# Kernel optimization log

Measured on AMD Instinct MI355X. Metric: run time of the kernel, lower is better.

## Reference

```python
import jax, jax.numpy as jnp
import numpy as np

N = 50000      # nodes
E = 250000     # edges
D = 256        # in_channels
MSG = 256      # msg_dim
TD = 64        # time encoder out_channels
ED = MSG + TD  # edge_dim = 320
H = 4          # heads
C = 64         # out_channels // heads


def setup_inputs() -> dict:
    key = jax.random.key(0)
    ks = jax.random.split(key, 16)
    s_d = 1.0 / np.sqrt(D)
    s_e = 1.0 / np.sqrt(ED)
    return {
        "x": jax.random.normal(ks[0], (N, D), jnp.float32),
        "last_update": jax.random.uniform(ks[1], (N,), jnp.float32) * 1000.0,
        "t": jax.random.uniform(ks[2], (E,), jnp.float32) * 1000.0,
        "msg": jax.random.normal(ks[3], (E, MSG), jnp.float32),
        "edge_index": jax.random.randint(ks[4], (2, E), 0, N, jnp.int32),
        # TimeEncoder: Linear(1, TD) followed by cos
        "time_w": jax.random.normal(ks[5], (TD,), jnp.float32),
        "time_b": jax.random.normal(ks[6], (TD,), jnp.float32) * 0.1,
        # TransformerConv linears (weights stored [out, in] like torch)
        "Wq": jax.random.normal(ks[7], (H * C, D), jnp.float32) * s_d,
        "bq": jnp.zeros((H * C,), jnp.float32),
        "Wk": jax.random.normal(ks[8], (H * C, D), jnp.float32) * s_d,
        "bk": jnp.zeros((H * C,), jnp.float32),
        "Wv": jax.random.normal(ks[9], (H * C, D), jnp.float32) * s_d,
        "bv": jnp.zeros((H * C,), jnp.float32),
        "We": jax.random.normal(ks[10], (H * C, ED), jnp.float32) * s_e,  # lin_edge, no bias
        "Wskip": jax.random.normal(ks[11], (H * C, D), jnp.float32) * s_d,
        "bskip": jnp.zeros((H * C,), jnp.float32),
    }


def reference(x, last_update, t, msg, edge_index, time_w, time_b,
              Wq, bq, Wk, bk, Wv, bv, We, Wskip, bskip):
    src = edge_index[0]  # j: message source
    dst = edge_index[1]  # i: message target

    # time encoding: cos(Linear(1, TD)(rel_t))
    rel_t = last_update[src] - t                              # [E]
    rel_t_enc = jnp.cos(rel_t[:, None] * time_w[None, :] + time_b)  # [E, TD]
    edge_attr = jnp.concatenate([rel_t_enc, msg], axis=-1)    # [E, ED]

    # TransformerConv (heads=4, concat=True, root_weight=True, beta=False, eval mode)
    q = (x @ Wq.T + bq).reshape(N, H, C)
    k = (x @ Wk.T + bk).reshape(N, H, C)
    v = (x @ Wv.T + bv).reshape(N, H, C)
    e = (edge_attr @ We.T).reshape(E, H, C)

    k_j = k[src] + e                                           # [E, H, C]
    alpha = jnp.einsum('ehc,ehc->eh', q[dst], k_j) / np.sqrt(C)  # [E, H]

    # segment softmax over incoming edges of each target node
    m = jax.ops.segment_max(alpha, dst, num_segments=N)        # [N, H]
    m = jnp.where(jnp.isfinite(m), m, 0.0)
    ex = jnp.exp(alpha - m[dst])                               # [E, H]
    denom = jax.ops.segment_sum(ex, dst, num_segments=N)       # [N, H]
    alpha = ex / (denom[dst] + 1e-16)                          # [E, H]

    out_e = (v[src] + e) * alpha[:, :, None]                   # [E, H, C]
    out = jax.ops.segment_sum(out_e, dst, num_segments=N)      # [N, H, C]
    out = out.reshape(N, H * C) + (x @ Wskip.T + bskip)        # skip connection
    return out
```

## Files before the change

### kernel.cpp

```cpp
#include <hip/hip_runtime.h>
#include <math.h>

#define NN 50000
#define EE 250000

typedef float f32x4 __attribute__((ext_vector_type(4)));
typedef __bf16 bf16x8 __attribute__((ext_vector_type(8)));

static __device__ __forceinline__ ushort f2b(float f) {
    __bf16 h = (__bf16)f;
    return *(ushort*)&h;
}
static __device__ __forceinline__ float b2f(ushort u) {
    return __uint_as_float(((unsigned)u) << 16);
}

typedef __attribute__((address_space(1))) const unsigned int gu32;
typedef __attribute__((address_space(3))) unsigned int lu32;
static __device__ __forceinline__ void gl2lds16(const void* g, void* l) {
    __builtin_amdgcn_global_load_lds((gu32*)g, (lu32*)l, 16, 0, 0);
}

__global__ void k_prep_w(const float* __restrict__ Wq, const float* __restrict__ bq,
                         const float* __restrict__ Wk, const float* __restrict__ bk,
                         const float* __restrict__ Wv, const float* __restrict__ bv,
                         const float* __restrict__ Wskip, const float* __restrict__ bskip,
                         const float* __restrict__ We,
                         ushort* __restrict__ Wnb_sw, ushort* __restrict__ Web_sw,
                         float* __restrict__ bcat) {
    int i = blockIdx.x * 256 + threadIdx.x;
    int st = gridDim.x * 256;
    for (int ch = i; ch < 16 * 2048; ch += st) {
        int tile = ch >> 11, pc = ch & 2047;
        int r = pc >> 5, sc = pc & 31;
        int c = (sc & 24) | ((sc ^ r) & 7);
        int n = tile * 64 + r, sel = n >> 8, o = n & 255;
        const float* W = (sel == 0) ? Wq : (sel == 1) ? Wk : (sel == 2) ? Wv : Wskip;
        const float* src = W + o * 256 + c * 8;
        union { ushort u[8]; uint4 v; } s;
        #pragma unroll
        for (int j = 0; j < 8; ++j) s.u[j] = f2b(src[j]);
        *(uint4*)&Wnb_sw[(size_t)ch * 8] = s.v;
    }
    for (int ch = i; ch < 5 * 2048; ch += st) {
        int ks = ch >> 11, pc = ch & 2047;
        int r = pc >> 3, q = pc & 7;
        int c = q ^ (r & 7);
        const float* src = We + r * 320 + ks * 64 + c * 8;
        union { ushort u[8]; uint4 v; } s;
        #pragma unroll
        for (int j = 0; j < 8; ++j) s.u[j] = f2b(src[j]);
        *(uint4*)&Web_sw[(size_t)ch * 8] = s.v;
    }
    for (int idx = i; idx < 1024; idx += st) {
        int sel = idx >> 8, o = idx & 255;
        const float* b = (sel == 0) ? bq : (sel == 1) ? bk : (sel == 2) ? bv : bskip;
        bcat[idx] = b[o];
    }
}

__global__ void k_zero(unsigned* __restrict__ deg) {
    int i = blockIdx.x * 256 + threadIdx.x;
    if (i < NN) deg[i] = 0u;
}

__global__ void k_hist(const int* __restrict__ ei, unsigned* __restrict__ deg) {
    int i = blockIdx.x * 256 + threadIdx.x;
    if (i < EE) atomicAdd(&deg[ei[EE + i]], 1u);
}

__global__ __launch_bounds__(1024) void k_scan(const unsigned* __restrict__ deg,
                                               unsigned* __restrict__ offs,
                                               unsigned* __restrict__ cursor) {
    __shared__ unsigned part[1024];
    int t = threadIdx.x;
    const int CH = (NN + 1023) / 1024;
    int b0 = t * CH;
    unsigned s = 0;
    for (int i = 0; i < CH; ++i) { int idx = b0 + i; if (idx < NN) s += deg[idx]; }
    part[t] = s;
    __syncthreads();
    for (int d = 1; d < 1024; d <<= 1) {
        unsigned v = (t >= d) ? part[t - d] : 0u;
        __syncthreads();
        part[t] += v;
        __syncthreads();
    }
    unsigned run = (t == 0) ? 0u : part[t - 1];
    for (int i = 0; i < CH; ++i) {
        int idx = b0 + i;
        if (idx < NN) { offs[idx] = run; cursor[idx] = run; run += deg[idx]; }
    }
    if (t == 1023) offs[NN] = EE;
}

__global__ void k_scatter(const int* __restrict__ ei, unsigned* __restrict__ cursor,
                          int* __restrict__ rank) {
    int i = blockIdx.x * 256 + threadIdx.x;
    if (i < EE) {
        unsigned p = atomicAdd(&cursor[ei[EE + i]], 1u);
        rank[i] = (int)p;
    }
}

__global__ __launch_bounds__(256) void k_node_mfma(
        const float* __restrict__ x, const ushort* __restrict__ Wnb_sw,
        const float* __restrict__ bcat,
        ushort* __restrict__ qb, ushort* __restrict__ kb, ushort* __restrict__ vb,
        float* __restrict__ out) {
    __shared__ ushort As[64 * 256];
    __shared__ ushort Bs[64 * 256];
    int tid = threadIdx.x;
    int lane = tid & 63, wid = tid >> 6;
    int wrow = wid >> 1, wcol = wid & 1;
    int li = lane & 15, g = lane >> 4;
    int bm = blockIdx.x, bng = blockIdx.y;
    #pragma unroll
    for (int i = 0; i < 8; ++i) {
        int ch = tid + i * 256;
        int r = ch >> 5, c = ch & 31;
        int row = bm * 64 + r;
        union { ushort u[8]; uint4 v; } s;
        if (row < NN) {
            const float* xr = x + (size_t)row * 256 + c * 8;
            float4 a = *(const float4*)xr;
            float4 b = *(const float4*)(xr + 4);
            s.u[0] = f2b(a.x); s.u[1] = f2b(a.y); s.u[2] = f2b(a.z); s.u[3] = f2b(a.w);
            s.u[4] = f2b(b.x); s.u[5] = f2b(b.y); s.u[6] = f2b(b.z); s.u[7] = f2b(b.w);
        } else {
            s.v = make_uint4(0, 0, 0, 0);
        }
        int sc = (c & 24) | ((c ^ r) & 7);
        *(uint4*)&As[r * 256 + sc * 8] = s.v;
    }
    for (int bn = 0; bn < 8; ++bn) {
        int bng2 = bng * 8 + bn;
        __syncthreads();
        #pragma unroll
        for (int i = 0; i < 8; ++i) {
            int pcb = (i * 4 + wid) * 64;
            gl2lds16(Wnb_sw + ((size_t)bng2 * 2048 + pcb + lane) * 8, &Bs[pcb * 8]);
        }
        __syncthreads();
        f32x4 acc[2][2] = {};
        #pragma unroll
        for (int ks = 0; ks < 8; ++ks) {
            bf16x8 a[2], b[2];
            int c = ks * 4 + g;
            #pragma unroll
            for (int m = 0; m < 2; ++m) {
                int r = wrow * 32 + m * 16 + li;
                int sc = (c & 24) | ((c ^ r) & 7);
                a[m] = *(const bf16x8*)&As[r * 256 + sc * 8];
            }
            #pragma unroll
            for (int n = 0; n < 2; ++n) {
                int r = wcol * 32 + n * 16 + li;
                int sc = (c & 24) | ((c ^ r) & 7);
                b[n] = *(const bf16x8*)&Bs[r * 256 + sc * 8];
            }
            #pragma unroll
            for (int m = 0; m < 2; ++m)
                #pragma unroll
                for (int n = 0; n < 2; ++n)
                    acc[m][n] = __builtin_amdgcn_mfma_f32_16x16x32_bf16(a[m], b[n], acc[m][n], 0, 0, 0);
        }
        int sel = bng2 >> 2;
        int cbase = (bng2 & 3) * 64;
        ushort* dstb = (sel == 0) ? qb : (sel == 1) ? kb : vb;
        #pragma unroll
        for (int m = 0; m < 2; ++m) {
            #pragma unroll
            for (int r = 0; r < 4; ++r) {
                int row = bm * 64 + wrow * 32 + m * 16 + g * 4 + r;
                if (row >= NN) continue;
                #pragma unroll
                for (int n = 0; n < 2; ++n) {
                    int coll = wcol * 32 + n * 16 + li;
                    float val = acc[m][n][r] + bcat[bng2 * 64 + coll];
                    int cin = cbase + coll;
                    if (sel < 3) dstb[(size_t)row * 256 + cin] = f2b(val);
                    else         out[(size_t)row * 256 + cin] = val;
                }
            }
        }
    }
}

__global__ __launch_bounds__(256) void k_edge_mfma(
        const float* __restrict__ msg, const float* __restrict__ t_arr,
        const float* __restrict__ lu, const float* __restrict__ tw,
        const float* __restrict__ tb, const ushort* __restrict__ Web_sw,
        const ushort* __restrict__ qb, const ushort* __restrict__ kb,
        const ushort* __restrict__ vb, const int* __restrict__ ei,
        const int* __restrict__ rank,
        ushort* __restrict__ ebuf, float* __restrict__ alpha) {
    __shared__ ushort SS[64 * 328];
    __shared__ int s_src[64], s_dst[64], s_rank[64];
    __shared__ float s_relt[64];
    int tid = threadIdx.x;
    int lane = tid & 63, wid = tid >> 6;
    int wr = wid >> 1, wc = wid & 1;
    int li = lane & 15, g = lane >> 4;
    int e0 = blockIdx.x * 64;
    if (tid < 64) {
        int e = e0 + tid;
        if (e >= EE) e = EE - 1;
        int s = ei[e];
        s_src[tid] = s;
        s_dst[tid] = ei[EE + e];
        s_rank[tid] = rank[e];
        s_relt[tid] = lu[s] - t_arr[e];
    }
    f32x4 acc[2][8] = {};
    for (int ks = 0; ks < 5; ++ks) {
        int k0 = ks * 64;
        __syncthreads();
        #pragma unroll
        for (int i = 0; i < 8; ++i) {
            int pcb = (i * 4 + wid) * 64;
            gl2lds16(Web_sw + ((size_t)ks * 2048 + pcb + lane) * 8, &SS[4096 + pcb * 8]);
        }
        #pragma unroll
        for (int i = 0; i < 2; ++i) {
            int ch = tid + i * 256;
            int r = ch >> 3, c = ch & 7;
            union { ushort u[8]; uint4 v; } s;
            if (k0 == 0) {
                float rt = s_relt[r];
                #pragma unroll
                for (int j = 0; j < 8; ++j)
                    s.u[j] = f2b(cosf(rt * tw[c * 8 + j] + tb[c * 8 + j]));
            } else {
                int erow = e0 + r; if (erow >= EE) erow = EE - 1;
                const float* mrow = msg + (size_t)erow * 256 + (k0 - 64) + c * 8;
                float4 a = *(const float4*)mrow;
                float4 b = *(const float4*)(mrow + 4);
                s.u[0] = f2b(a.x); s.u[1] = f2b(a.y); s.u[2] = f2b(a.z); s.u[3] = f2b(a.w);
                s.u[4] = f2b(b.x); s.u[5] = f2b(b.y); s.u[6] = f2b(b.z); s.u[7] = f2b(b.w);
            }
            *(uint4*)&SS[r * 64 + ((c ^ (r & 7)) * 8)] = s.v;
        }
        __syncthreads();
        #pragma unroll
        for (int kk = 0; kk < 2; ++kk) {
            bf16x8 a[2], b[8];
            #pragma unroll
            for (int m = 0; m < 2; ++m) {
                int r = wr * 32 + m * 16 + li;
                a[m] = *(const bf16x8*)&SS[r * 64 + (((kk * 4 + g) ^ (r & 7)) * 8)];
            }
            #pragma unroll
            for (int n = 0; n < 8; ++n) {
                int r = wc * 128 + n * 16 + li;
                b[n] = *(const bf16x8*)&SS[4096 + r * 64 + (((kk * 4 + g) ^ (r & 7)) * 8)];
            }
            #pragma unroll
            for (int m = 0; m < 2; ++m)
                #pragma unroll
                for (int n = 0; n < 8; ++n)
                    acc[m][n] = __builtin_amdgcn_mfma_f32_16x16x32_bf16(a[m], b[n], acc[m][n], 0, 0, 0);
        }
    }
    __syncthreads();
    #pragma unroll
    for (int i = 0; i < 8; ++i) {
        int idx = tid + i * 256;
        int r = idx >> 5, c = idx & 31;
        uint4 vv = *(const uint4*)(vb + (size_t)s_src[r] * 256 + c * 8);
        *(uint4*)&SS[r * 328 + c * 8] = vv;
    }
    __syncthreads();
    #pragma unroll
    for (int m = 0; m < 2; ++m) {
        #pragma unroll
        for (int r = 0; r < 4; ++r) {
            int el = wr * 32 + m * 16 + g * 4 + r;
            int edge = e0 + el;
            if (edge >= EE) continue;
            size_t rb = (size_t)s_rank[el] * 256;
            #pragma unroll
            for (int n = 0; n < 8; ++n) {
                int col = wc * 128 + n * 16 + li;
                ebuf[rb + col] = f2b(acc[m][n][r] + b2f(SS[el * 328 + col]));
            }
        }
    }
    __syncthreads();
    #pragma unroll
    for (int i = 0; i < 8; ++i) {
        int idx = tid + i * 256;
        int r = idx >> 5, c = idx & 31;
        uint4 kv = *(const uint4*)(kb + (size_t)s_src[r] * 256 + c * 8);
        *(uint4*)&SS[r * 328 + c * 8] = kv;
    }
    __syncthreads();
    #pragma unroll
    for (int m = 0; m < 2; ++m)
        #pragma unroll
        for (int r = 0; r < 4; ++r) {
            int el = wr * 32 + m * 16 + g * 4 + r;
            #pragma unroll
            for (int n = 0; n < 8; ++n)
                acc[m][n][r] += b2f(SS[el * 328 + wc * 128 + n * 16 + li]);
        }
    __syncthreads();
    #pragma unroll
    for (int i = 0; i < 8; ++i) {
        int idx = tid + i * 256;
        int r = idx >> 5, c = idx & 31;
        uint4 qv = *(const uint4*)(qb + (size_t)s_dst[r] * 256 + c * 8);
        *(uint4*)&SS[r * 328 + c * 8] = qv;
    }
    __syncthreads();
    #pragma unroll
    for (int m = 0; m < 2; ++m) {
        #pragma unroll
        for (int r = 0; r < 4; ++r) {
            int el = wr * 32 + m * 16 + g * 4 + r;
            int edge = e0 + el;
            float p0 = 0.f, p1 = 0.f;
            #pragma unroll
            for (int n = 0; n < 8; ++n) {
                float qv = b2f(SS[el * 328 + wc * 128 + n * 16 + li]);
                float tt = qv * acc[m][n][r];
                if (n < 4) p0 += tt; else p1 += tt;
            }
            #pragma unroll
            for (int msk = 1; msk < 16; msk <<= 1) {
                p0 += __shfl_xor(p0, msk);
                p1 += __shfl_xor(p1, msk);
            }
            if (li < 2 && edge < EE) {
                float av = ((li == 0) ? p0 : p1) * 0.125f;
                int h = wc * 2 + li;
                alpha[(size_t)s_rank[el] * 4 + h] = av;
            }
        }
    }
}

__global__ __launch_bounds__(256) void k_gather(
        const ushort* __restrict__ ebuf, const float* __restrict__ alpha,
        const unsigned* __restrict__ offs, float* __restrict__ out) {
    int wid = threadIdx.x >> 6, lane = threadIdx.x & 63;
    int n = blockIdx.x * 4 + wid;
    if (n >= NN) return;
    unsigned p0 = offs[n], p1 = offs[n + 1];
    if (p0 == p1) return;
    int h = lane >> 4;
    int c0 = lane * 4;
    float m = -INFINITY;
    for (unsigned p = p0; p < p1; ++p)
        m = fmaxf(m, alpha[(size_t)p * 4 + h]);
    f32x4 acc = {0.f, 0.f, 0.f, 0.f};
    float denom = 0.f;
    for (unsigned p = p0; p < p1; ++p) {
        float ex = __expf(alpha[(size_t)p * 4 + h] - m);
        ushort4 ev = *(const ushort4*)(ebuf + (size_t)p * 256 + c0);
        acc[0] += b2f(ev.x) * ex;
        acc[1] += b2f(ev.y) * ex;
        acc[2] += b2f(ev.z) * ex;
        acc[3] += b2f(ev.w) * ex;
        denom += ex;
    }
    float inv = 1.f / (denom + 1e-16f);
    float4 o = *(float4*)(out + (size_t)n * 256 + c0);
    o.x += acc[0] * inv;
    o.y += acc[1] * inv;
    o.z += acc[2] * inv;
    o.w += acc[3] * inv;
    *(float4*)(out + (size_t)n * 256 + c0) = o;
}

extern "C" void kernel_launch(void* const* d_in, const int* in_sizes, int n_in,
                              void* d_out, int out_size, void* d_ws, size_t ws_size,
                              hipStream_t stream) {
    const float* x        = (const float*)d_in[0];
    const float* last_upd = (const float*)d_in[1];
    const float* t_arr    = (const float*)d_in[2];
    const float* msg      = (const float*)d_in[3];
    const int*   ei       = (const int*)d_in[4];
    const float* time_w   = (const float*)d_in[5];
    const float* time_b   = (const float*)d_in[6];
    const float* Wq = (const float*)d_in[7];  const float* bq = (const float*)d_in[8];
    const float* Wk = (const float*)d_in[9];  const float* bk = (const float*)d_in[10];
    const float* Wv = (const float*)d_in[11]; const float* bv = (const float*)d_in[12];
    const float* We = (const float*)d_in[13];
    const float* Wsk = (const float*)d_in[14]; const float* bsk = (const float*)d_in[15];
    float* out = (float*)d_out;
    char* base = (char*)d_ws;

    size_t off = 0;
    auto carve = [&](size_t bytes) {
        void* p = base + off;
        off += (bytes + 255) & ~(size_t)255;
        return p;
    };
    ushort* Wnb_sw = (ushort*)carve((size_t)16 * 2048 * 8 * 2);
    ushort* Web_sw = (ushort*)carve((size_t)5 * 2048 * 8 * 2);
    float*  bcat  = (float*) carve(1024 * 4);
    ushort* qb    = (ushort*)carve((size_t)NN * 256 * 2);
    ushort* kb    = (ushort*)carve((size_t)NN * 256 * 2);
    ushort* vb    = (ushort*)carve((size_t)NN * 256 * 2);
    ushort* ebuf  = (ushort*)carve((size_t)EE * 256 * 2);
    float*  alpha = (float*) carve((size_t)EE * 4 * 4);
    unsigned* deg    = (unsigned*)carve((size_t)NN * 4);
    unsigned* cursor = (unsigned*)carve((size_t)NN * 4);
    unsigned* offs   = (unsigned*)carve((size_t)(NN + 1) * 4);
    int*      rank   = (int*)     carve((size_t)EE * 4);

    k_prep_w<<<dim3(512), dim3(256), 0, stream>>>(Wq, bq, Wk, bk, Wv, bv, Wsk, bsk, We,
                                                  Wnb_sw, Web_sw, bcat);
    k_zero<<<dim3((NN + 255) / 256), dim3(256), 0, stream>>>(deg);
    k_hist<<<dim3((EE + 255) / 256), dim3(256), 0, stream>>>(ei, deg);
    k_scan<<<dim3(1), dim3(1024), 0, stream>>>(deg, offs, cursor);
    k_scatter<<<dim3((EE + 255) / 256), dim3(256), 0, stream>>>(ei, cursor, rank);
    k_node_mfma<<<dim3(782, 2), dim3(256), 0, stream>>>(x, Wnb_sw, bcat, qb, kb, vb, out);
    k_edge_mfma<<<dim3((EE + 63) / 64), dim3(256), 0, stream>>>(
        msg, t_arr, last_upd, time_w, time_b, Web_sw, qb, kb, vb, ei, rank, ebuf, alpha);
    k_gather<<<dim3((NN + 3) / 4), dim3(256), 0, stream>>>(ebuf, alpha, offs, out);
}
```

Baseline: 555.7 us.

## Shrink edge kernel LDS via 32-wide K steps and half-tile gather epilogue

The edge MFMA kernel now steps K in chunks of 32 instead of 64, with the We weight layout and XOR swizzle reworked to match. The epilogue gathers v/k/q rows for 32 edges at a time rather than 64, and only the owning warps consume each half. Together these cut the shared-memory footprint from about 42KB to about 20KB, so more blocks can be resident per CU. The cost is twice as many K-loop barriers and a serialized two-pass epilogue in which half the warps sit idle during each pass.

```diff
diff --git a/kernel.cpp b/kernel.cpp
--- a/kernel.cpp
+++ b/kernel.cpp
@@ -42,11 +42,11 @@
         for (int j = 0; j < 8; ++j) s.u[j] = f2b(src[j]);
         *(uint4*)&Wnb_sw[(size_t)ch * 8] = s.v;
     }
-    for (int ch = i; ch < 5 * 2048; ch += st) {
-        int ks = ch >> 11, pc = ch & 2047;
-        int r = pc >> 3, q = pc & 7;
-        int c = q ^ (r & 7);
-        const float* src = We + r * 320 + ks * 64 + c * 8;
+    for (int ch = i; ch < 10 * 1024; ch += st) {
+        int ks = ch >> 10, pc = ch & 1023;
+        int r = pc >> 2, sc = pc & 3;
+        int c = sc ^ ((r >> 2) & 3);
+        const float* src = We + r * 320 + ks * 32 + c * 8;
         union { ushort u[8]; uint4 v; } s;
         #pragma unroll
         for (int j = 0; j < 8; ++j) s.u[j] = f2b(src[j]);
@@ -195,7 +195,7 @@
         const ushort* __restrict__ vb, const int* __restrict__ ei,
         const int* __restrict__ rank,
         ushort* __restrict__ ebuf, float* __restrict__ alpha) {
-    __shared__ ushort SS[64 * 328];
+    __shared__ ushort SS[10240];
     __shared__ int s_src[64], s_dst[64], s_rank[64];
     __shared__ float s_relt[64];
     int tid = threadIdx.x;
@@ -213,24 +213,23 @@
         s_relt[tid] = lu[s] - t_arr[e];
     }
     f32x4 acc[2][8] = {};
-    for (int ks = 0; ks < 5; ++ks) {
-        int k0 = ks * 64;
-        __syncthreads();
-        #pragma unroll
-        for (int i = 0; i < 8; ++i) {
+    for (int ks = 0; ks < 10; ++ks) {
+        int k0 = ks * 32;
+        __syncthreads();
+        #pragma unroll
+        for (int i = 0; i < 4; ++i) {
             int pcb = (i * 4 + wid) * 64;
-            gl2lds16(Web_sw + ((size_t)ks * 2048 + pcb + lane) * 8, &SS[4096 + pcb * 8]);
-        }
-        #pragma unroll
-        for (int i = 0; i < 2; ++i) {
-            int ch = tid + i * 256;
-            int r = ch >> 3, c = ch & 7;
+            gl2lds16(Web_sw + ((size_t)ks * 1024 + pcb + lane) * 8,
+                     &SS[2048 + pcb * 8]);
+        }
+        {
+            int r = tid >> 2, c = tid & 3;
             union { ushort u[8]; uint4 v; } s;
-            if (k0 == 0) {
+            if (k0 < 64) {
                 float rt = s_relt[r];
                 #pragma unroll
                 for (int j = 0; j < 8; ++j)
-                    s.u[j] = f2b(cosf(rt * tw[c * 8 + j] + tb[c * 8 + j]));
+                    s.u[j] = f2b(cosf(rt * tw[k0 + c * 8 + j] + tb[k0 + c * 8 + j]));
             } else {
                 int erow = e0 + r; if (erow >= EE) erow = EE - 1;
                 const float* mrow = msg + (size_t)erow * 256 + (k0 - 64) + c * 8;
@@ -239,102 +238,110 @@
                 s.u[0] = f2b(a.x); s.u[1] = f2b(a.y); s.u[2] = f2b(a.z); s.u[3] = f2b(a.w);
                 s.u[4] = f2b(b.x); s.u[5] = f2b(b.y); s.u[6] = f2b(b.z); s.u[7] = f2b(b.w);
             }
-            *(uint4*)&SS[r * 64 + ((c ^ (r & 7)) * 8)] = s.v;
-        }
-        __syncthreads();
-        #pragma unroll
-        for (int kk = 0; kk < 2; ++kk) {
-            bf16x8 a[2], b[8];
+            int sc = c ^ ((r >> 2) & 3);
+            *(uint4*)&SS[r * 32 + sc * 8] = s.v;
+        }
+        __syncthreads();
+        bf16x8 a[2], b[8];
+        #pragma unroll
+        for (int m = 0; m < 2; ++m) {
+            int r = wr * 32 + m * 16 + li;
+            a[m] = *(const bf16x8*)&SS[r * 32 + ((g ^ ((r >> 2) & 3)) * 8)];
+        }
+        #pragma unroll
+        for (int n = 0; n < 8; ++n) {
+            int r = wc * 128 + n * 16 + li;
+            b[n] = *(const bf16x8*)&SS[2048 + r * 32 + ((g ^ ((r >> 2) & 3)) * 8)];
+        }
+        #pragma unroll
+        for (int m = 0; m < 2; ++m)
+            #pragma unroll
+            for (int n = 0; n < 8; ++n)
+                acc[m][n] = __builtin_amdgcn_mfma_f32_16x16x32_bf16(a[m], b[n], acc[m][n], 0, 0, 0);
+    }
+    #pragma unroll
+    for (int hh = 0; hh < 2; ++hh) {
+        bool own = (wr == hh);
+        __syncthreads();
+        #pragma unroll
+        for (int i = 0; i < 4; ++i) {
+            int idx = tid + i * 256;
+            int r = idx >> 5, c = idx & 31;
+            uint4 vv = *(const uint4*)(vb + (size_t)s_src[hh * 32 + r] * 256 + c * 8);
+            *(uint4*)&SS[r * 264 + c * 8] = vv;
+        }
+        __syncthreads();
+        if (own) {
             #pragma unroll
             for (int m = 0; m < 2; ++m) {
-                int r = wr * 32 + m * 16 + li;
-                a[m] = *(const bf16x8*)&SS[r * 64 + (((kk * 4 + g) ^ (r & 7)) * 8)];
-            }
-            #pragma unroll
-            for (int n = 0; n < 8; ++n) {
-                int r = wc * 128 + n * 16 + li;
-                b[n] = *(const bf16x8*)&SS[4096 + r * 64 + (((kk * 4 + g) ^ (r & 7)) * 8)];
-            }
+                #pragma unroll
+                for (int r = 0; r < 4; ++r) {
+                    int el = m * 16 + g * 4 + r;
+                    int edge = e0 + hh * 32 + el;
+                    if (edge >= EE) continue;
+                    size_t rb = (size_t)s_rank[hh * 32 + el] * 256;
+                    #pragma unroll
+                    for (int n = 0; n < 8; ++n) {
+                        int col = wc * 128 + n * 16 + li;
+                        ebuf[rb + col] = f2b(acc[m][n][r] + b2f(SS[el * 264 + col]));
+                    }
+                }
+            }
+        }
+        __syncthreads();
+        #pragma unroll
+        for (int i = 0; i < 4; ++i) {
+            int idx = tid + i * 256;
+            int r = idx >> 5, c = idx & 31;
+            uint4 kv = *(const uint4*)(kb + (size_t)s_src[hh * 32 + r] * 256 + c * 8);
+            *(uint4*)&SS[r * 264 + c * 8] = kv;
+        }
+        __syncthreads();
+        if (own) {
             #pragma unroll
             for (int m = 0; m < 2; ++m)
                 #pragma unroll
-                for (int n = 0; n < 8; ++n)
-                    acc[m][n] = __builtin_amdgcn_mfma_f32_16x16x32_bf16(a[m], b[n], acc[m][n], 0, 0, 0);
-        }
-    }
-    __syncthreads();
-    #pragma unroll
-    for (int i = 0; i < 8; ++i) {
-        int idx = tid + i * 256;
-        int r = idx >> 5, c = idx & 31;
-        uint4 vv = *(const uint4*)(vb + (size_t)s_src[r] * 256 + c * 8);
-        *(uint4*)&SS[r * 328 + c * 8] = vv;
-    }
-    __syncthreads();
-    #pragma unroll
-    for (int m = 0; m < 2; ++m) {
-        #pragma unroll
-        for (int r = 0; r < 4; ++r) {
-            int el = wr * 32 + m * 16 + g * 4 + r;
-            int edge = e0 + el;
-            if (edge >= EE) continue;
-            size_t rb = (size_t)s_rank[el] * 256;
-            #pragma unroll
-            for (int n = 0; n < 8; ++n) {
-                int col = wc * 128 + n * 16 + li;
-                ebuf[rb + col] = f2b(acc[m][n][r] + b2f(SS[el * 328 + col]));
-            }
-        }
-    }
-    __syncthreads();
-    #pragma unroll
-    for (int i = 0; i < 8; ++i) {
-        int idx = tid + i * 256;
-        int r = idx >> 5, c = idx & 31;
-        uint4 kv = *(const uint4*)(kb + (size_t)s_src[r] * 256 + c * 8);
-        *(uint4*)&SS[r * 328 + c * 8] = kv;
-    }
-    __syncthreads();
-    #pragma unroll
-    for (int m = 0; m < 2; ++m)
-        #pragma unroll
-        for (int r = 0; r < 4; ++r) {
-            int el = wr * 32 + m * 16 + g * 4 + r;
-            #pragma unroll
-            for (int n = 0; n < 8; ++n)
-                acc[m][n][r] += b2f(SS[el * 328 + wc * 128 + n * 16 + li]);
-        }
-    __syncthreads();
-    #pragma unroll
-    for (int i = 0; i < 8; ++i) {
-        int idx = tid + i * 256;
-        int r = idx >> 5, c = idx & 31;
-        uint4 qv = *(const uint4*)(qb + (size_t)s_dst[r] * 256 + c * 8);
-        *(uint4*)&SS[r * 328 + c * 8] = qv;
-    }
-    __syncthreads();
-    #pragma unroll
-    for (int m = 0; m < 2; ++m) {
-        #pragma unroll
-        for (int r = 0; r < 4; ++r) {
-            int el = wr * 32 + m * 16 + g * 4 + r;
-            int edge = e0 + el;
-            float p0 = 0.f, p1 = 0.f;
-            #pragma unroll
-            for (int n = 0; n < 8; ++n) {
-                float qv = b2f(SS[el * 328 + wc * 128 + n * 16 + li]);
-                float tt = qv * acc[m][n][r];
-                if (n < 4) p0 += tt; else p1 += tt;
-            }
-            #pragma unroll
-            for (int msk = 1; msk < 16; msk <<= 1) {
-                p0 += __shfl_xor(p0, msk);
-                p1 += __shfl_xor(p1, msk);
-            }
-            if (li < 2 && edge < EE) {
-                float av = ((li == 0) ? p0 : p1) * 0.125f;
-                int h = wc * 2 + li;
-                alpha[(size_t)s_rank[el] * 4 + h] = av;
+                for (int r = 0; r < 4; ++r) {
+                    int el = m * 16 + g * 4 + r;
+                    #pragma unroll
+                    for (int n = 0; n < 8; ++n)
+                        acc[m][n][r] += b2f(SS[el * 264 + wc * 128 + n * 16 + li]);
+                }
+        }
+        __syncthreads();
+        #pragma unroll
+        for (int i = 0; i < 4; ++i) {
+            int idx = tid + i * 256;
+            int r = idx >> 5, c = idx & 31;
+            uint4 qv = *(const uint4*)(qb + (size_t)s_dst[hh * 32 + r] * 256 + c * 8);
+            *(uint4*)&SS[r * 264 + c * 8] = qv;
+        }
+        __syncthreads();
+        if (own) {
+            #pragma unroll
+            for (int m = 0; m < 2; ++m) {
+                #pragma unroll
+                for (int r = 0; r < 4; ++r) {
+                    int el = m * 16 + g * 4 + r;
+                    int edge = e0 + hh * 32 + el;
+                    float p0 = 0.f, p1 = 0.f;
+                    #pragma unroll
+                    for (int n = 0; n < 8; ++n) {
+                        float qv = b2f(SS[el * 264 + wc * 128 + n * 16 + li]);
+                        float tt = qv * acc[m][n][r];
+                        if (n < 4) p0 += tt; else p1 += tt;
+                    }
+                    #pragma unroll
+                    for (int msk = 1; msk < 16; msk <<= 1) {
+                        p0 += __shfl_xor(p0, msk);
+                        p1 += __shfl_xor(p1, msk);
+                    }
+                    if (li < 2 && edge < EE) {
+                        float av = ((li == 0) ? p0 : p1) * 0.125f;
+                        int h = wc * 2 + li;
+                        alpha[(size_t)s_rank[hh * 32 + el] * 4 + h] = av;
+                    }
+                }
             }
         }
     }
@@ -398,7 +405,7 @@
         return p;
     };
     ushort* Wnb_sw = (ushort*)carve((size_t)16 * 2048 * 8 * 2);
-    ushort* Web_sw = (ushort*)carve((size_t)5 * 2048 * 8 * 2);
+    ushort* Web_sw = (ushort*)carve((size_t)10 * 1024 * 8 * 2);
     float*  bcat  = (float*) carve(1024 * 4);
     ushort* qb    = (ushort*)carve((size_t)NN * 256 * 2);
     ushort* kb    = (ushort*)carve((size_t)NN * 256 * 2);
```

After: 587.4 us. 5.7% more time.

## Process edges in destination-sorted order and fold degree zeroing into prep

Applied to the files above, without the earlier changes.

The scatter pass now writes per-edge src, dst, original id and relative time into CSR-sorted arrays, so the edge kernel walks edges in destination order. Its ebuf and alpha writes become contiguous, and the q[dst] gathers hit nearby rows. In exchange, msg rows are now read by a scattered original edge id, and the scatter pass writes four arrays instead of one. The separate zeroing kernel is merged into the weight prep kernel to save a launch.

```diff
diff --git a/kernel.cpp b/kernel.cpp
--- a/kernel.cpp
+++ b/kernel.cpp
@@ -27,7 +27,7 @@
                          const float* __restrict__ Wskip, const float* __restrict__ bskip,
                          const float* __restrict__ We,
                          ushort* __restrict__ Wnb_sw, ushort* __restrict__ Web_sw,
-                         float* __restrict__ bcat) {
+                         float* __restrict__ bcat, unsigned* __restrict__ deg) {
     int i = blockIdx.x * 256 + threadIdx.x;
     int st = gridDim.x * 256;
     for (int ch = i; ch < 16 * 2048; ch += st) {
@@ -57,11 +57,7 @@
         const float* b = (sel == 0) ? bq : (sel == 1) ? bk : (sel == 2) ? bv : bskip;
         bcat[idx] = b[o];
     }
-}
-
-__global__ void k_zero(unsigned* __restrict__ deg) {
-    int i = blockIdx.x * 256 + threadIdx.x;
-    if (i < NN) deg[i] = 0u;
+    for (int idx = i; idx < NN; idx += st) deg[idx] = 0u;
 }
 
 __global__ void k_hist(const int* __restrict__ ei, unsigned* __restrict__ deg) {
@@ -94,12 +90,18 @@
     if (t == 1023) offs[NN] = EE;
 }
 
-__global__ void k_scatter(const int* __restrict__ ei, unsigned* __restrict__ cursor,
-                          int* __restrict__ rank) {
+__global__ void k_scatter(const int* __restrict__ ei, const float* __restrict__ t_arr,
+                          const float* __restrict__ lu, unsigned* __restrict__ cursor,
+                          int* __restrict__ s_srcA, int* __restrict__ s_dstA,
+                          float* __restrict__ s_reltA, int* __restrict__ s_eidA) {
     int i = blockIdx.x * 256 + threadIdx.x;
     if (i < EE) {
-        unsigned p = atomicAdd(&cursor[ei[EE + i]], 1u);
-        rank[i] = (int)p;
+        int s = ei[i], d = ei[EE + i];
+        unsigned p = atomicAdd(&cursor[d], 1u);
+        s_srcA[p] = s;
+        s_dstA[p] = d;
+        s_eidA[p] = i;
+        s_reltA[p] = lu[s] - t_arr[i];
     }
 }
 
@@ -188,15 +190,15 @@
 }
 
 __global__ __launch_bounds__(256) void k_edge_mfma(
-        const float* __restrict__ msg, const float* __restrict__ t_arr,
-        const float* __restrict__ lu, const float* __restrict__ tw,
+        const float* __restrict__ msg, const float* __restrict__ tw,
         const float* __restrict__ tb, const ushort* __restrict__ Web_sw,
         const ushort* __restrict__ qb, const ushort* __restrict__ kb,
-        const ushort* __restrict__ vb, const int* __restrict__ ei,
-        const int* __restrict__ rank,
+        const ushort* __restrict__ vb,
+        const int* __restrict__ s_srcA, const int* __restrict__ s_dstA,
+        const float* __restrict__ s_reltA, const int* __restrict__ s_eidA,
         ushort* __restrict__ ebuf, float* __restrict__ alpha) {
     __shared__ ushort SS[64 * 328];
-    __shared__ int s_src[64], s_dst[64], s_rank[64];
+    __shared__ int s_src[64], s_dst[64], s_eid[64];
     __shared__ float s_relt[64];
     int tid = threadIdx.x;
     int lane = tid & 63, wid = tid >> 6;
@@ -204,13 +206,12 @@
     int li = lane & 15, g = lane >> 4;
     int e0 = blockIdx.x * 64;
     if (tid < 64) {
-        int e = e0 + tid;
-        if (e >= EE) e = EE - 1;
-        int s = ei[e];
-        s_src[tid] = s;
-        s_dst[tid] = ei[EE + e];
-        s_rank[tid] = rank[e];
-        s_relt[tid] = lu[s] - t_arr[e];
+        int p = e0 + tid;
+        if (p >= EE) p = EE - 1;
+        s_src[tid] = s_srcA[p];
+        s_dst[tid] = s_dstA[p];
+        s_eid[tid] = s_eidA[p];
+        s_relt[tid] = s_reltA[p];
     }
     f32x4 acc[2][8] = {};
     for (int ks = 0; ks < 5; ++ks) {
@@ -232,8 +233,7 @@
                 for (int j = 0; j < 8; ++j)
                     s.u[j] = f2b(cosf(rt * tw[c * 8 + j] + tb[c * 8 + j]));
             } else {
-                int erow = e0 + r; if (erow >= EE) erow = EE - 1;
-                const float* mrow = msg + (size_t)erow * 256 + (k0 - 64) + c * 8;
+                const float* mrow = msg + (size_t)s_eid[r] * 256 + (k0 - 64) + c * 8;
                 float4 a = *(const float4*)mrow;
                 float4 b = *(const float4*)(mrow + 4);
                 s.u[0] = f2b(a.x); s.u[1] = f2b(a.y); s.u[2] = f2b(a.z); s.u[3] = f2b(a.w);
@@ -276,9 +276,9 @@
         #pragma unroll
         for (int r = 0; r < 4; ++r) {
             int el = wr * 32 + m * 16 + g * 4 + r;
-            int edge = e0 + el;
-            if (edge >= EE) continue;
-            size_t rb = (size_t)s_rank[el] * 256;
+            int p = e0 + el;
+            if (p >= EE) continue;
+            size_t rb = (size_t)p * 256;
             #pragma unroll
             for (int n = 0; n < 8; ++n) {
                 int col = wc * 128 + n * 16 + li;
@@ -318,7 +318,7 @@
         #pragma unroll
         for (int r = 0; r < 4; ++r) {
             int el = wr * 32 + m * 16 + g * 4 + r;
-            int edge = e0 + el;
+            int p = e0 + el;
             float p0 = 0.f, p1 = 0.f;
             #pragma unroll
             for (int n = 0; n < 8; ++n) {
@@ -331,10 +331,10 @@
                 p0 += __shfl_xor(p0, msk);
                 p1 += __shfl_xor(p1, msk);
             }
-            if (li < 2 && edge < EE) {
+            if (li < 2 && p < EE) {
                 float av = ((li == 0) ? p0 : p1) * 0.125f;
                 int h = wc * 2 + li;
-                alpha[(size_t)s_rank[el] * 4 + h] = av;
+                alpha[(size_t)p * 4 + h] = av;
             }
         }
     }
@@ -408,16 +408,20 @@
     unsigned* deg    = (unsigned*)carve((size_t)NN * 4);
     unsigned* cursor = (unsigned*)carve((size_t)NN * 4);
     unsigned* offs   = (unsigned*)carve((size_t)(NN + 1) * 4);
-    int*      rank   = (int*)     carve((size_t)EE * 4);
+    int*      s_srcA = (int*)    carve((size_t)EE * 4);
+    int*      s_dstA = (int*)    carve((size_t)EE * 4);
+    float*    s_reltA= (float*)  carve((size_t)EE * 4);
+    int*      s_eidA = (int*)    carve((size_t)EE * 4);
 
     k_prep_w<<<dim3(512), dim3(256), 0, stream>>>(Wq, bq, Wk, bk, Wv, bv, Wsk, bsk, We,
-                                                  Wnb_sw, Web_sw, bcat);
-    k_zero<<<dim3((NN + 255) / 256), dim3(256), 0, stream>>>(deg);
+                                                  Wnb_sw, Web_sw, bcat, deg);
     k_hist<<<dim3((EE + 255) / 256), dim3(256), 0, stream>>>(ei, deg);
     k_scan<<<dim3(1), dim3(1024), 0, stream>>>(deg, offs, cursor);
-    k_scatter<<<dim3((EE + 255) / 256), dim3(256), 0, stream>>>(ei, cursor, rank);
+    k_scatter<<<dim3((EE + 255) / 256), dim3(256), 0, stream>>>(
+        ei, t_arr, last_upd, cursor, s_srcA, s_dstA, s_reltA, s_eidA);
     k_node_mfma<<<dim3(782, 2), dim3(256), 0, stream>>>(x, Wnb_sw, bcat, qb, kb, vb, out);
     k_edge_mfma<<<dim3((EE + 63) / 64), dim3(256), 0, stream>>>(
-        msg, t_arr, last_upd, time_w, time_b, Web_sw, qb, kb, vb, ei, rank, ebuf, alpha);
+        msg, time_w, time_b, Web_sw, qb, kb, vb,
+        s_srcA, s_dstA, s_reltA, s_eidA, ebuf, alpha);
     k_gather<<<dim3((NN + 3) / 4), dim3(256), 0, stream>>>(ebuf, alpha, offs, out);
 }
```

Result: slower. 655.7 us (+18.0%).

## Split edge kernel into pure GEMM and separate gather epilogue kernel

Applied to the files above, without the earlier changes.

The fused edge kernel is split into two launches. The first is a GEMM-only kernel that writes the raw edge projection in bf16, laid out in edge order. The second is a wave-per-edge epilogue that gathers q, k and v, writes e+v in rank order and computes the attention logits. The aim is to shrink the GEMM kernel's LDS use and remove its serialized gather phases to improve occupancy, at the cost of an extra 128MB intermediate buffer round trip and one more launch. The degree zeroing is also folded into the weight prep kernel to drop one launch.

```diff
diff --git a/kernel.cpp b/kernel.cpp
--- a/kernel.cpp
+++ b/kernel.cpp
@@ -27,7 +27,7 @@
                          const float* __restrict__ Wskip, const float* __restrict__ bskip,
                          const float* __restrict__ We,
                          ushort* __restrict__ Wnb_sw, ushort* __restrict__ Web_sw,
-                         float* __restrict__ bcat) {
+                         float* __restrict__ bcat, unsigned* __restrict__ deg) {
     int i = blockIdx.x * 256 + threadIdx.x;
     int st = gridDim.x * 256;
     for (int ch = i; ch < 16 * 2048; ch += st) {
@@ -57,11 +57,7 @@
         const float* b = (sel == 0) ? bq : (sel == 1) ? bk : (sel == 2) ? bv : bskip;
         bcat[idx] = b[o];
     }
-}
-
-__global__ void k_zero(unsigned* __restrict__ deg) {
-    int i = blockIdx.x * 256 + threadIdx.x;
-    if (i < NN) deg[i] = 0u;
+    for (int idx = i; idx < NN; idx += st) deg[idx] = 0u;
 }
 
 __global__ void k_hist(const int* __restrict__ ei, unsigned* __restrict__ deg) {
@@ -187,16 +183,12 @@
     }
 }
 
-__global__ __launch_bounds__(256) void k_edge_mfma(
+__global__ __launch_bounds__(256) void k_edge_gemm(
         const float* __restrict__ msg, const float* __restrict__ t_arr,
         const float* __restrict__ lu, const float* __restrict__ tw,
         const float* __restrict__ tb, const ushort* __restrict__ Web_sw,
-        const ushort* __restrict__ qb, const ushort* __restrict__ kb,
-        const ushort* __restrict__ vb, const int* __restrict__ ei,
-        const int* __restrict__ rank,
-        ushort* __restrict__ ebuf, float* __restrict__ alpha) {
-    __shared__ ushort SS[64 * 328];
-    __shared__ int s_src[64], s_dst[64], s_rank[64];
+        const int* __restrict__ ei, ushort* __restrict__ ebuf_raw) {
+    __shared__ ushort SS[20480];
     __shared__ float s_relt[64];
     int tid = threadIdx.x;
     int lane = tid & 63, wid = tid >> 6;
@@ -206,11 +198,7 @@
     if (tid < 64) {
         int e = e0 + tid;
         if (e >= EE) e = EE - 1;
-        int s = ei[e];
-        s_src[tid] = s;
-        s_dst[tid] = ei[EE + e];
-        s_rank[tid] = rank[e];
-        s_relt[tid] = lu[s] - t_arr[e];
+        s_relt[tid] = lu[ei[e]] - t_arr[e];
     }
     f32x4 acc[2][8] = {};
     for (int ks = 0; ks < 5; ++ks) {
@@ -262,15 +250,6 @@
                     acc[m][n] = __builtin_amdgcn_mfma_f32_16x16x32_bf16(a[m], b[n], acc[m][n], 0, 0, 0);
         }
     }
-    __syncthreads();
-    #pragma unroll
-    for (int i = 0; i < 8; ++i) {
-        int idx = tid + i * 256;
-        int r = idx >> 5, c = idx & 31;
-        uint4 vv = *(const uint4*)(vb + (size_t)s_src[r] * 256 + c * 8);
-        *(uint4*)&SS[r * 328 + c * 8] = vv;
-    }
-    __syncthreads();
     #pragma unroll
     for (int m = 0; m < 2; ++m) {
         #pragma unroll
@@ -278,66 +257,45 @@
             int el = wr * 32 + m * 16 + g * 4 + r;
             int edge = e0 + el;
             if (edge >= EE) continue;
-            size_t rb = (size_t)s_rank[el] * 256;
             #pragma unroll
             for (int n = 0; n < 8; ++n) {
                 int col = wc * 128 + n * 16 + li;
-                ebuf[rb + col] = f2b(acc[m][n][r] + b2f(SS[el * 328 + col]));
-            }
-        }
-    }
-    __syncthreads();
+                ebuf_raw[(size_t)edge * 256 + col] = f2b(acc[m][n][r]);
+            }
+        }
+    }
+}
+
+__global__ __launch_bounds__(256) void k_edge_epi(
+        const ushort* __restrict__ ebuf_raw, const ushort* __restrict__ qb,
+        const ushort* __restrict__ kb, const ushort* __restrict__ vb,
+        const int* __restrict__ ei, const int* __restrict__ rank,
+        ushort* __restrict__ ebuf, float* __restrict__ alpha) {
+    int wid = threadIdx.x >> 6, lane = threadIdx.x & 63;
+    int e = blockIdx.x * 4 + wid;
+    if (e >= EE) return;
+    int src = ei[e], dst = ei[EE + e];
+    int rk = rank[e];
+    int c0 = lane * 4;
+    ushort4 ev = *(const ushort4*)(ebuf_raw + (size_t)e * 256 + c0);
+    ushort4 vv = *(const ushort4*)(vb + (size_t)src * 256 + c0);
+    ushort4 kv = *(const ushort4*)(kb + (size_t)src * 256 + c0);
+    ushort4 qv = *(const ushort4*)(qb + (size_t)dst * 256 + c0);
+    float e0f = b2f(ev.x), e1f = b2f(ev.y), e2f = b2f(ev.z), e3f = b2f(ev.w);
+    ushort4 ov;
+    ov.x = f2b(e0f + b2f(vv.x));
+    ov.y = f2b(e1f + b2f(vv.y));
+    ov.z = f2b(e2f + b2f(vv.z));
+    ov.w = f2b(e3f + b2f(vv.w));
+    *(ushort4*)(ebuf + (size_t)rk * 256 + c0) = ov;
+    float part = b2f(qv.x) * (b2f(kv.x) + e0f)
+               + b2f(qv.y) * (b2f(kv.y) + e1f)
+               + b2f(qv.z) * (b2f(kv.z) + e2f)
+               + b2f(qv.w) * (b2f(kv.w) + e3f);
     #pragma unroll
-    for (int i = 0; i < 8; ++i) {
-        int idx = tid + i * 256;
-        int r = idx >> 5, c = idx & 31;
-        uint4 kv = *(const uint4*)(kb + (size_t)s_src[r] * 256 + c * 8);
-        *(uint4*)&SS[r * 328 + c * 8] = kv;
-    }
-    __syncthreads();
-    #pragma unroll
-    for (int m = 0; m < 2; ++m)
-        #pragma unroll
-        for (int r = 0; r < 4; ++r) {
-            int el = wr * 32 + m * 16 + g * 4 + r;
-            #pragma unroll
-            for (int n = 0; n < 8; ++n)
-                acc[m][n][r] += b2f(SS[el * 328 + wc * 128 + n * 16 + li]);
-        }
-    __syncthreads();
-    #pragma unroll
-    for (int i = 0; i < 8; ++i) {
-        int idx = tid + i * 256;
-        int r = idx >> 5, c = idx & 31;
-        uint4 qv = *(const uint4*)(qb + (size_t)s_dst[r] * 256 + c * 8);
-        *(uint4*)&SS[r * 328 + c * 8] = qv;
-    }
-    __syncthreads();
-    #pragma unroll
-    for (int m = 0; m < 2; ++m) {
-        #pragma unroll
-        for (int r = 0; r < 4; ++r) {
-            int el = wr * 32 + m * 16 + g * 4 + r;
-            int edge = e0 + el;
-            float p0 = 0.f, p1 = 0.f;
-            #pragma unroll
-            for (int n = 0; n < 8; ++n) {
-                float qv = b2f(SS[el * 328 + wc * 128 + n * 16 + li]);
-                float tt = qv * acc[m][n][r];
-                if (n < 4) p0 += tt; else p1 += tt;
-            }
-            #pragma unroll
-            for (int msk = 1; msk < 16; msk <<= 1) {
-                p0 += __shfl_xor(p0, msk);
-                p1 += __shfl_xor(p1, msk);
-            }
-            if (li < 2 && edge < EE) {
-                float av = ((li == 0) ? p0 : p1) * 0.125f;
-                int h = wc * 2 + li;
-                alpha[(size_t)s_rank[el] * 4 + h] = av;
-            }
-        }
-    }
+    for (int msk = 1; msk < 16; msk <<= 1) part += __shfl_xor(part, msk);
+    if ((lane & 15) == 0)
+        alpha[(size_t)rk * 4 + (lane >> 4)] = part * 0.125f;
 }
 
 __global__ __launch_bounds__(256) void k_gather(
@@ -403,6 +361,7 @@
     ushort* qb    = (ushort*)carve((size_t)NN * 256 * 2);
     ushort* kb    = (ushort*)carve((size_t)NN * 256 * 2);
     ushort* vb    = (ushort*)carve((size_t)NN * 256 * 2);
+    ushort* ebuf_raw = (ushort*)carve((size_t)EE * 256 * 2);
     ushort* ebuf  = (ushort*)carve((size_t)EE * 256 * 2);
     float*  alpha = (float*) carve((size_t)EE * 4 * 4);
     unsigned* deg    = (unsigned*)carve((size_t)NN * 4);
@@ -411,13 +370,14 @@
     int*      rank   = (int*)     carve((size_t)EE * 4);
 
     k_prep_w<<<dim3(512), dim3(256), 0, stream>>>(Wq, bq, Wk, bk, Wv, bv, Wsk, bsk, We,
-                                                  Wnb_sw, Web_sw, bcat);
-    k_zero<<<dim3((NN + 255) / 256), dim3(256), 0, stream>>>(deg);
+                                                  Wnb_sw, Web_sw, bcat, deg);
     k_hist<<<dim3((EE + 255) / 256), dim3(256), 0, stream>>>(ei, deg);
     k_scan<<<dim3(1), dim3(1024), 0, stream>>>(deg, offs, cursor);
     k_scatter<<<dim3((EE + 255) / 256), dim3(256), 0, stream>>>(ei, cursor, rank);
     k_node_mfma<<<dim3(782, 2), dim3(256), 0, stream>>>(x, Wnb_sw, bcat, qb, kb, vb, out);
-    k_edge_mfma<<<dim3((EE + 63) / 64), dim3(256), 0, stream>>>(
-        msg, t_arr, last_upd, time_w, time_b, Web_sw, qb, kb, vb, ei, rank, ebuf, alpha);
+    k_edge_gemm<<<dim3((EE + 63) / 64), dim3(256), 0, stream>>>(
+        msg, t_arr, last_upd, time_w, time_b, Web_sw, ei, ebuf_raw);
+    k_edge_epi<<<dim3((EE + 3) / 4), dim3(256), 0, stream>>>(
+        ebuf_raw, qb, kb, vb, ei, rank, ebuf, alpha);
     k_gather<<<dim3((NN + 3) / 4), dim3(256), 0, stream>>>(ebuf, alpha, offs, out);
 }
```

Measured after the change: 584.4 us. 5.2% more time.
